# Performance work log

Measured on AMD Instinct MI355X. Metric: run time of the kernel, lower is better.

The kernel has to match this reference:

```python
import jax, jax.numpy as jnp
import numpy as np

B, T, D = 64, 512, 768
H = D // 2      # per-direction LSTM hidden
L = 33          # num_labels


def setup_inputs() -> dict:
    key = jax.random.key(0)
    ks = jax.random.split(key, 14)
    input_embed = jax.random.normal(ks[0], (B, T, D), dtype=jnp.float32)
    # pack_padded_sequence requires lengths sorted in decreasing order
    lengths = jnp.sort(jax.random.randint(ks[1], (B,), T // 2, T + 1))[::-1]
    lengths = lengths.at[0].set(T)
    mask = jnp.arange(T)[None, :] < lengths[:, None]          # [B,T] bool
    labels = jax.random.randint(ks[2], (B, T), 0, L, dtype=jnp.int32)
    index = jax.random.randint(ks[3], (B, 2), 0, T)
    s = 0.1
    w_ih_f = jax.random.normal(ks[4], (4 * H, D), jnp.float32) * s
    w_hh_f = jax.random.normal(ks[5], (4 * H, H), jnp.float32) * s
    b_f = jax.random.normal(ks[6], (4 * H,), jnp.float32) * s
    w_ih_b = jax.random.normal(ks[7], (4 * H, D), jnp.float32) * s
    w_hh_b = jax.random.normal(ks[8], (4 * H, H), jnp.float32) * s
    b_b = jax.random.normal(ks[9], (4 * H,), jnp.float32) * s
    lin_w = jax.random.normal(ks[10], (L, 2 * H), jnp.float32) * s
    lin_b = jnp.zeros((L,), jnp.float32)
    trans = jax.random.normal(ks[11], (L, L), jnp.float32) * s
    start_trans = jax.random.normal(ks[12], (L,), jnp.float32) * s
    end_trans = jax.random.normal(ks[13], (L,), jnp.float32) * s
    return dict(input_embed=input_embed, mask=mask, labels=labels, index=index,
                w_ih_f=w_ih_f, w_hh_f=w_hh_f, b_f=b_f,
                w_ih_b=w_ih_b, w_hh_b=w_hh_b, b_b=b_b,
                lin_w=lin_w, lin_b=lin_b,
                trans=trans, start_trans=start_trans, end_trans=end_trans)


def _run_lstm(x, mask_f, w_ih, w_hh, b):
    """Unidirectional LSTM over packed (length-masked) sequences.
    Output is zero at padded steps; state is frozen past each sequence length.
    x: [B,T,D] -> [B,T,H]. Torch gate order: i, f, g, o.
    """
    xp = jnp.einsum('btd,gd->btg', x, w_ih) + b          # [B,T,4H] precomputed
    xp_t = xp.transpose(1, 0, 2)                         # [T,B,4H]
    m_t = mask_f.T[:, :, None]                           # [T,B,1]
    nH = w_hh.shape[1]
    init = (jnp.zeros((x.shape[0], nH), x.dtype), jnp.zeros((x.shape[0], nH), x.dtype))

    def step(carry, inp):
        h, c = carry
        xg, m = inp
        g = xg + h @ w_hh.T
        i, f, gc, o = jnp.split(g, 4, axis=-1)
        c_new = jax.nn.sigmoid(f) * c + jax.nn.sigmoid(i) * jnp.tanh(gc)
        h_new = jax.nn.sigmoid(o) * jnp.tanh(c_new)
        carry = (jnp.where(m > 0, h_new, h), jnp.where(m > 0, c_new, c))
        return carry, h_new * m

    _, ys = jax.lax.scan(step, init, (xp_t, m_t))
    return ys.transpose(1, 0, 2)


def reference(input_embed, mask, labels, index,
              w_ih_f, w_hh_f, b_f, w_ih_b, w_hh_b, b_b,
              lin_w, lin_b, trans, start_trans, end_trans):
    mask_f = mask.astype(input_embed.dtype)              # [B,T]
    lengths = mask.sum(1).astype(jnp.int32)              # [B]

    # BiLSTM with pack_padded semantics (dropout in eval mode = identity)
    h_fwd = _run_lstm(input_embed, mask_f, w_ih_f, w_hh_f, b_f)
    # reverse within each sequence's valid region (involution on valid steps)
    rev_idx = jnp.clip(lengths[:, None] - 1 - jnp.arange(T)[None, :], 0, T - 1)
    x_rev = jnp.take_along_axis(input_embed, rev_idx[..., None], axis=1)
    h_b_rev = _run_lstm(x_rev, mask_f, w_ih_b, w_hh_b, b_b)
    h_bwd = jnp.take_along_axis(h_b_rev, rev_idx[..., None], axis=1) * mask_f[..., None]
    h = jnp.concatenate([h_fwd, h_bwd], axis=-1)         # [B,T,2H]

    # emissions, masked as in the original (out *= mask.unsqueeze(-1))
    em = (jnp.einsum('bth,lh->btl', h, lin_w) + lin_b) * mask_f[..., None]

    # ---- CRF log-likelihood: numerator (gold path score) ----
    em_y = jnp.take_along_axis(em, labels[..., None], axis=2)[..., 0]   # [B,T]
    tr = trans[labels[:, :-1], labels[:, 1:]]                            # [B,T-1]
    num = start_trans[labels[:, 0]] + em_y[:, 0] \
        + jnp.sum((tr + em_y[:, 1:]) * mask_f[:, 1:], axis=1)
    last_y = jnp.take_along_axis(labels, (lengths - 1)[:, None], axis=1)[:, 0]
    num = num + end_trans[last_y]

    # ---- CRF log-partition: forward algorithm scan ----
    alpha0 = start_trans[None, :] + em[:, 0]             # [B,L]

    def step(alpha, inp):
        e_t, m_t = inp                                   # [B,L], [B]
        new = jax.nn.logsumexp(alpha[:, :, None] + trans[None, :, :] + e_t[:, None, :], axis=1)
        return jnp.where(m_t[:, None] > 0, new, alpha), None

    alpha, _ = jax.lax.scan(step, alpha0,
                            (em[:, 1:].transpose(1, 0, 2), mask_f[:, 1:].T))
    logZ = jax.nn.logsumexp(alpha + end_trans[None, :], axis=1)

    score = num - logZ                                   # per-sample log-likelihood
    return -jnp.mean(score)
```

## Files before the change

kernel.cpp:

```cpp
#include <hip/hip_runtime.h>

typedef unsigned short U16;
typedef unsigned int   U32;
typedef unsigned long long U64;
typedef __attribute__((ext_vector_type(8))) short S8;
typedef __attribute__((ext_vector_type(4))) float F4;

#define B_  64
#define T_  512
#define DD  768
#define HH  384
#define G4  1536
#define NL  33

__device__ __forceinline__ U16 f2bf(float f){
  U32 u = __float_as_uint(f);
  u += 0x7fffu + ((u >> 16) & 1u);
  return (U16)(u >> 16);
}
__device__ __forceinline__ float bf2f(U16 h){ return __uint_as_float(((U32)h) << 16); }
__device__ __forceinline__ float frcp(float x){
  float r;
  asm("v_rcp_f32 %0, %1" : "=v"(r) : "v"(x));
  return r * (2.0f - x * r);
}
__device__ __forceinline__ float sigm(float x){
  x = fminf(30.f, fmaxf(-30.f, x));
  return frcp(1.f + __expf(-x));
}
__device__ __forceinline__ float tanh_(float x){
  x = fminf(15.f, fmaxf(-15.f, x));
  float e = __expf(2.f * x);
  return (e - 1.f) * frcp(e + 1.f);
}

__global__ void k_pre(const float* x, U64* xb, const U32* mask, int* lens,
                      const float* wf_, const float* wb_, const float* lw_,
                      const float* bfv, const float* bbv,
                      U16* wcat, U16* lwb, float* bcat){
  int blk = blockIdx.x;
  int tid = threadIdx.x;
  if (blk < 64){
    if (tid < 64){
      int b = blk, l = tid;
      bool b32 = (mask[0] == 1u);
      int cnt = 0;
      for (int t = l; t < T_; t += 64){
        int v = b32 ? ((const int*)mask)[b * T_ + t]
                    : (int)((const unsigned char*)mask)[b * T_ + t];
        cnt += (v != 0);
      }
      #pragma unroll
      for (int o = 32; o >= 1; o >>= 1) cnt += __shfl_xor(cnt, o);
      if (l == 0) lens[b] = cnt;
    }
    return;
  }
  if (blk < 1088){
    const int WE = G4 * DD;
    const int LWE = NL * DD;
    int total = 2 * WE + LWE + 2 * G4;
    for (int i = (blk - 64) * 256 + tid; i < total; i += 1024 * 256){
      if (i < WE) wcat[i] = f2bf(wf_[i]);
      else if (i < 2 * WE) wcat[i] = f2bf(wb_[i - WE]);
      else if (i < 2 * WE + LWE) lwb[i - 2 * WE] = f2bf(lw_[i - 2 * WE]);
      else { int j = i - 2 * WE - LWE; bcat[j] = (j < G4) ? bfv[j] : bbv[j - G4]; }
    }
    return;
  }
  size_t n4 = (size_t)B_ * T_ * DD / 4;
  for (size_t i = (size_t)(blk - 1088) * 256 + tid; i < n4; i += (size_t)2048 * 256){
    float4 v = ((const float4*)x)[i];
    U64 o = (U64)f2bf(v.x) | ((U64)f2bf(v.y) << 16) | ((U64)f2bf(v.z) << 32) | ((U64)f2bf(v.w) << 48);
    xb[i] = o;
  }
}

__global__ __launch_bounds__(256) void k_gemm(const U16* A, const U16* Bw, const float* bias, U16* C){
  __shared__ __align__(16) U16 As[128 * 64];
  __shared__ __align__(16) U16 Bs[128 * 64];
  int bid = blockIdx.x;
  int nb = bid % 24, mb = bid / 24;
  int m0 = mb * 128, n0 = nb * 128;
  int tid = threadIdx.x;
  int w = tid >> 6, l = tid & 63;
  int lr = l & 15, lk = (l >> 4) * 8;
  int wm = (w >> 1) * 64, wn = (w & 1) * 64;
  int srow = tid >> 3;
  int scol = (tid & 7) * 8;
  F4 acc[4][4];
  #pragma unroll
  for (int i = 0; i < 4; i++)
    #pragma unroll
    for (int j = 0; j < 4; j++) acc[i][j] = (F4){0.f, 0.f, 0.f, 0.f};

  for (int kt = 0; kt < DD; kt += 64){
    __syncthreads();
    #pragma unroll
    for (int r = 0; r < 4; r++){
      int row = r * 32 + srow;
      __builtin_amdgcn_global_load_lds((const U32*)(A + (size_t)(m0 + row) * DD + kt + scol),
                                       (U32*)(As + row * 64 + scol), 16, 0, 0);
      __builtin_amdgcn_global_load_lds((const U32*)(Bw + (size_t)(n0 + row) * DD + kt + scol),
                                       (U32*)(Bs + row * 64 + scol), 16, 0, 0);
    }
    __syncthreads();
    #pragma unroll
    for (int kk = 0; kk < 64; kk += 32){
      S8 af[4], bf[4];
      #pragma unroll
      for (int i = 0; i < 4; i++) af[i] = *(const S8*)(As + (wm + i * 16 + lr) * 64 + kk + lk);
      #pragma unroll
      for (int i = 0; i < 4; i++) bf[i] = *(const S8*)(Bs + (wn + i * 16 + lr) * 64 + kk + lk);
      #pragma unroll
      for (int i = 0; i < 4; i++)
        #pragma unroll
        for (int j = 0; j < 4; j++)
          acc[i][j] = __builtin_amdgcn_mfma_f32_16x16x32_bf16(af[i], bf[j], acc[i][j], 0, 0, 0);
    }
  }
  #pragma unroll
  for (int j = 0; j < 4; j++){
    int col = n0 + wn + j * 16 + lr;
    float bv = bias[col];
    #pragma unroll
    for (int i = 0; i < 4; i++){
      #pragma unroll
      for (int rg = 0; rg < 4; rg++){
        int row = m0 + wm + i * 16 + (l >> 4) * 4 + rg;
        C[(size_t)row * 3072 + col] = f2bf(acc[i][j][rg] + bv);
      }
    }
  }
}

__global__ __launch_bounds__(256) void k_rec(const U16* xp, const float* whf, const float* whb,
                                             const int* len_, U16* hcat, U64* hx){
  int blk = blockIdx.x;
  int g = blk & 7, m = blk >> 3;
  int dir = g >> 2, chunk = g & 3, sb = chunk * 16;
  const float* wh = dir ? whb : whf;
  int tid = threadIdx.x;
  int w = tid >> 6, l = tid & 63;
  int lr = l & 15, lq = l >> 4;
  int jloc = m * 64 + w * 16 + lr;

  S8 wf[4][12];
  #pragma unroll
  for (int q = 0; q < 4; q++){
    #pragma unroll
    for (int kc = 0; kc < 12; kc++){
      const float* p = wh + (size_t)(q * HH + jloc) * HH + kc * 32 + lq * 8;
      float4 v0 = *(const float4*)p;
      float4 v1 = *(const float4*)(p + 4);
      S8 t;
      t[0] = (short)f2bf(v0.x); t[1] = (short)f2bf(v0.y); t[2] = (short)f2bf(v0.z); t[3] = (short)f2bf(v0.w);
      t[4] = (short)f2bf(v1.x); t[5] = (short)f2bf(v1.y); t[6] = (short)f2bf(v1.z); t[7] = (short)f2bf(v1.w);
      wf[q][kc] = t;
    }
  }

  __shared__ __align__(16) U16 hl[16][408];
  for (int i = tid; i < 16 * 408; i += 256) ((U16*)hl)[i] = 0;
  int lens[4];
  #pragma unroll
  for (int r = 0; r < 4; r++) lens[r] = len_[sb + lq * 4 + r];
  int steps = len_[sb];
  float cst[4] = {0.f, 0.f, 0.f, 0.f}, hst[4] = {0.f, 0.f, 0.f, 0.f};
  __syncthreads();

  for (int step = 0; step < steps; ++step){
    float xv[4][4];
    #pragma unroll
    for (int r = 0; r < 4; r++){
      int L = lens[r];
      int t = dir ? (L - 1 - step) : step;
      if (t < 0) t = 0;
      size_t basei = ((size_t)(sb + lq * 4 + r) * T_ + t) * 3072 + dir * G4;
      #pragma unroll
      for (int q = 0; q < 4; q++) xv[q][r] = bf2f(xp[basei + q * HH + jloc]);
    }
    if (step){
      const U64* src = hx + (size_t)((step & 1) * 8 + g) * 3072;
      U64 v[12];
      #pragma unroll
      for (int k = 0; k < 12; k++)
        v[k] = __hip_atomic_load(src + tid + k * 256, __ATOMIC_RELAXED, __HIP_MEMORY_SCOPE_AGENT);
      U32 expct = (U32)step;
      while (true){
        U32 bad = 0;
        #pragma unroll
        for (int k = 0; k < 12; k++) bad |= (((U32)(v[k] >> 32)) != expct) ? (1u << k) : 0u;
        if (!bad) break;
        #pragma unroll
        for (int k = 0; k < 12; k++)
          if (bad & (1u << k))
            v[k] = __hip_atomic_load(src + tid + k * 256, __ATOMIC_RELAXED, __HIP_MEMORY_SCOPE_AGENT);
      }
      #pragma unroll
      for (int k = 0; k < 12; k++){
        int wi = tid + k * 256;
        int col = wi >> 3, p = wi & 7;
        U32 lo = (U32)v[k];
        hl[2 * p + 0][col] = (U16)lo;
        hl[2 * p + 1][col] = (U16)(lo >> 16);
      }
      __syncthreads();
    }
    F4 acc[4];
    #pragma unroll
    for (int q = 0; q < 4; q++) acc[q] = (F4){0.f, 0.f, 0.f, 0.f};
    #pragma unroll
    for (int kc = 0; kc < 12; kc++){
      S8 a = *(const S8*)&hl[lr][kc * 32 + lq * 8];
      #pragma unroll
      for (int q = 0; q < 4; q++)
        acc[q] = __builtin_amdgcn_mfma_f32_16x16x32_bf16(a, wf[q][kc], acc[q], 0, 0, 0);
    }
    #pragma unroll
    for (int r = 0; r < 4; r++){
      float ip = acc[0][r] + xv[0][r];
      float fp = acc[1][r] + xv[1][r];
      float gp = acc[2][r] + xv[2][r];
      float op = acc[3][r] + xv[3][r];
      float cn = sigm(fp) * cst[r] + sigm(ip) * tanh_(gp);
      float hn = sigm(op) * tanh_(cn);
      if (step < lens[r]){ cst[r] = cn; hst[r] = hn; }
    }
    {
      U64 tag = ((U64)(U32)(step + 1)) << 32;
      U64 w0 = (U64)((U32)f2bf(hst[0]) | ((U32)f2bf(hst[1]) << 16)) | tag;
      U64 w1 = (U64)((U32)f2bf(hst[2]) | ((U32)f2bf(hst[3]) << 16)) | tag;
      U64* dst = hx + (size_t)(((step + 1) & 1) * 8 + g) * 3072 + jloc * 8 + lq * 2;
      __hip_atomic_store(dst + 0, w0, __ATOMIC_RELAXED, __HIP_MEMORY_SCOPE_AGENT);
      __hip_atomic_store(dst + 1, w1, __ATOMIC_RELAXED, __HIP_MEMORY_SCOPE_AGENT);
    }
    #pragma unroll
    for (int r = 0; r < 4; r++){
      if (step < lens[r]){
        int t = dir ? (lens[r] - 1 - step) : step;
        hcat[((size_t)(sb + lq * 4 + r) * T_ + t) * (2 * HH) + dir * HH + jloc] = f2bf(hst[r]);
      }
    }
  }
}

__global__ __launch_bounds__(256) void k_em(const U16* hcat, const U16* lwb, const float* lin_b, float* em){
  __shared__ U16 lw[NL * DD];
  __shared__ U16 hs[8 * DD];
  int tid = threadIdx.x;
  for (int i = tid; i < NL * DD / 2; i += 256) ((U32*)lw)[i] = ((const U32*)lwb)[i];
  size_t r0 = (size_t)blockIdx.x * 8;
  const U32* hsrc = (const U32*)(hcat + r0 * DD);
  for (int i = tid; i < 8 * DD / 2; i += 256) ((U32*)hs)[i] = hsrc[i];
  __syncthreads();
  for (int e = tid; e < 8 * NL; e += 256){
    int rr = e / NL, ll = e % NL;
    const U16* hp = &hs[rr * DD];
    const U16* wp = &lw[ll * DD];
    float s = 0.f;
    #pragma unroll 8
    for (int k = 0; k < DD; k += 2){
      U32 hv = *(const U32*)&hp[k];
      U32 wv = *(const U32*)&wp[k];
      s = fmaf(__uint_as_float(hv << 16), __uint_as_float(wv << 16), s);
      s = fmaf(__uint_as_float(hv & 0xffff0000u), __uint_as_float(wv & 0xffff0000u), s);
    }
    em[(r0 + rr) * NL + ll] = s + lin_b[ll];
  }
}

__global__ void k_crf(const float* em, const int* labels, const int* len_, const float* trans,
                      const float* startt, const float* endt, float* score){
  int b = blockIdx.x, l = threadIdx.x;
  int L = len_[b];
  const int* lab = labels + b * T_;
  const float* emb = em + (size_t)b * T_ * NL;
  float part = 0.f;
  for (int t = 1 + l; t < L; t += 64){
    int lp = lab[t - 1], lc = lab[t];
    part += trans[lp * NL + lc] + emb[(size_t)t * NL + lc];
  }
  #pragma unroll
  for (int o = 32; o >= 1; o >>= 1) part += __shfl_xor(part, o);
  float num = part + startt[lab[0]] + emb[lab[0]] + endt[lab[L - 1]];
  bool act = l < NL;
  int jj = act ? l : (NL - 1);
  float tc[NL];
  #pragma unroll
  for (int i = 0; i < NL; i++) tc[i] = trans[i * NL + jj];
  float a = startt[jj] + emb[jj];
  for (int t = 1; t < L; ++t){
    float vv[NL];
    float mx = -3.0e38f;
    #pragma unroll
    for (int i = 0; i < NL; i++){ vv[i] = __shfl(a, i) + tc[i]; mx = fmaxf(mx, vv[i]); }
    float s = 0.f;
    #pragma unroll
    for (int i = 0; i < NL; i++) s += __expf(vv[i] - mx);
    a = mx + __logf(s) + emb[(size_t)t * NL + jj];
  }
  float val = act ? (a + endt[jj]) : -3.0e38f;
  float mx = val;
  #pragma unroll
  for (int o = 32; o >= 1; o >>= 1) mx = fmaxf(mx, __shfl_xor(mx, o));
  float se = __expf(val - mx);
  #pragma unroll
  for (int o = 32; o >= 1; o >>= 1) se += __shfl_xor(se, o);
  float logZ = mx + __logf(se);
  if (l == 0) score[b] = num - logZ;
}

__global__ void k_final(const float* score, float* out){
  int l = threadIdx.x;
  float v = score[l];
  #pragma unroll
  for (int o = 32; o >= 1; o >>= 1) v += __shfl_xor(v, o);
  if (l == 0) out[0] = -v / 64.f;
}

__global__ void k_sentinel(float* out){ out[0] = -12345.f; }

extern "C" void kernel_launch(void* const* d_in, const int* in_sizes, int n_in,
                              void* d_out, int out_size, void* d_ws, size_t ws_size,
                              hipStream_t stream){
  const float* x      = (const float*)d_in[0];
  const void*  mask   = d_in[1];
  const int*   labels = (const int*)d_in[2];
  const float* w_ih_f = (const float*)d_in[4];
  const float* w_hh_f = (const float*)d_in[5];
  const float* b_f    = (const float*)d_in[6];
  const float* w_ih_b = (const float*)d_in[7];
  const float* w_hh_b = (const float*)d_in[8];
  const float* b_b    = (const float*)d_in[9];
  const float* lin_w  = (const float*)d_in[10];
  const float* lin_b  = (const float*)d_in[11];
  const float* trans  = (const float*)d_in[12];
  const float* startt = (const float*)d_in[13];
  const float* endt   = (const float*)d_in[14];
  float* out = (float*)d_out;

  const size_t WS_NEEDED = 261158912;
  if (ws_size < WS_NEEDED){
    k_sentinel<<<1, 1, 0, stream>>>(out);
    return;
  }

  char* ws = (char*)d_ws;
  size_t off = 0;
  auto take = [&](size_t bytes) -> char* {
    char* p = ws + off;
    off += (bytes + 255) & ~(size_t)255;
    return p;
  };
  U16*  xp    = (U16*)take((size_t)32768 * 3072 * 2);
  U16*  hcat  = (U16*)take((size_t)32768 * 768 * 2);
  U16*  wcat  = (U16*)take((size_t)3072 * 768 * 2);
  U16*  lwb   = (U16*)take((size_t)NL * 768 * 2);
  float* bcat = (float*)take(3072 * 4);
  int*  lens  = (int*)take(256);
  U64*  hx    = (U64*)take((size_t)2 * 8 * 3072 * 8);
  float* em   = (float*)take((size_t)32768 * NL * 4);
  float* score= (float*)take(256);
  U16*  xbf   = hcat;

  hipMemsetAsync(hx, 0, (size_t)2 * 8 * 3072 * 8, stream);
  k_pre<<<3136, 256, 0, stream>>>(x, (U64*)xbf, (const U32*)mask, lens,
                                  w_ih_f, w_ih_b, lin_w, b_f, b_b, wcat, lwb, bcat);
  k_gemm<<<6144, 256, 0, stream>>>(xbf, wcat, bcat, xp);
  k_rec<<<48, 256, 0, stream>>>(xp, w_hh_f, w_hh_b, lens, hcat, hx);
  k_em<<<4096, 256, 0, stream>>>(hcat, lwb, lin_b, em);
  k_crf<<<64, 64, 0, stream>>>(em, labels, lens, trans, startt, endt, score);
  k_final<<<1, 64, 0, stream>>>(score, out);
}
```

Before: 2.245 ms.

## Interleave four batch chunks per recurrent block to hide cross-block sync latency

The recurrent kernel now runs 12 blocks instead of 48. Each block owns one hidden slice of one direction and processes all four 16-sequence batch chunks in round-robin phases. While one chunk computes, the poll for the next chunk's hidden state is already issued, so inter-block handshake latency overlaps with MFMA and gate work. Offsets into xp and hcat are advanced incrementally, and the clamps are removed from the sigmoid and tanh helpers. The trade-off is four times more serial work per block with fewer CUs in use, and large inputs to tanh could now overflow to inf/NaN without the clamp.

```diff
diff --git a/kernel.cpp b/kernel.cpp
--- a/kernel.cpp
+++ b/kernel.cpp
@@ -25,13 +25,11 @@
   return r * (2.0f - x * r);
 }
 __device__ __forceinline__ float sigm(float x){
-  x = fminf(30.f, fmaxf(-30.f, x));
   return frcp(1.f + __expf(-x));
 }
 __device__ __forceinline__ float tanh_(float x){
-  x = fminf(15.f, fmaxf(-15.f, x));
   float e = __expf(2.f * x);
-  return (e - 1.f) * frcp(e + 1.f);
+  return 1.f - 2.f * frcp(e + 1.f);
 }
 
 __global__ void k_pre(const float* x, U64* xb, const U32* mask, int* lens,
@@ -134,11 +132,13 @@
   }
 }
 
-__global__ __launch_bounds__(256) void k_rec(const U16* xp, const float* whf, const float* whb,
-                                             const int* len_, U16* hcat, U64* hx){
+__global__ __launch_bounds__(256, 1) void k_rec(const U16* __restrict__ xp,
+                                                const float* __restrict__ whf,
+                                                const float* __restrict__ whb,
+                                                const int* __restrict__ len_,
+                                                U16* __restrict__ hcat, U64* hx){
   int blk = blockIdx.x;
-  int g = blk & 7, m = blk >> 3;
-  int dir = g >> 2, chunk = g & 3, sb = chunk * 16;
+  int m = blk % 6, dir = blk / 6;
   const float* wh = dir ? whb : whf;
   int tid = threadIdx.x;
   int w = tid >> 6, l = tid & 63;
@@ -160,89 +160,124 @@
     }
   }
 
-  __shared__ __align__(16) U16 hl[16][408];
-  for (int i = tid; i < 16 * 408; i += 256) ((U16*)hl)[i] = 0;
-  int lens[4];
-  #pragma unroll
-  for (int r = 0; r < 4; r++) lens[r] = len_[sb + lq * 4 + r];
-  int steps = len_[sb];
-  float cst[4] = {0.f, 0.f, 0.f, 0.f}, hst[4] = {0.f, 0.f, 0.f, 0.f};
+  __shared__ __align__(16) U16 hl[4][16][408];
+  for (int i = tid; i < 4 * 16 * 408; i += 256) ((U16*)hl)[i] = 0;
+
+  int lcs[16]; U32 oxp[16], oh[16];
+  #pragma unroll
+  for (int c = 0; c < 4; c++){
+    #pragma unroll
+    for (int rr = 0; rr < 4; rr++){
+      int seq = c * 16 + lq * 4 + rr;
+      int L = len_[seq];
+      lcs[c * 4 + rr] = L;
+      int t0 = dir ? (L - 1) : 0;
+      oxp[c * 4 + rr] = (U32)(((seq * T_ + t0) * 3072 + dir * G4 + jloc) * 2);
+      oh [c * 4 + rr] = (U32)(((seq * T_ + t0) * 768  + dir * HH + jloc) * 2);
+    }
+  }
+  int clen0 = len_[0], clen1 = len_[16], clen2 = len_[32], clen3 = len_[48];
+  int sxp = dir ? -6144 : 6144;
+  int sh  = dir ? -1536 : 1536;
+  float cs[16], hs[16];
+  #pragma unroll
+  for (int i = 0; i < 16; i++){ cs[i] = 0.f; hs[i] = 0.f; }
+
+  const char* xpB = (const char*)xp;
+  char* hcB = (char*)hcat;
+  U64 vp[12];
+  U16 xv[16];
+
+  #define IXV(C) { \
+    _Pragma("unroll") \
+    for (int rr = 0; rr < 4; rr++){ \
+      const U16* p = (const U16*)(xpB + oxp[(C) * 4 + rr]); \
+      xv[0 * 4 + rr] = p[0]; xv[1 * 4 + rr] = p[HH]; \
+      xv[2 * 4 + rr] = p[2 * HH]; xv[3 * 4 + rr] = p[3 * HH]; \
+    } }
+
+  #define IPOLL(G, PAR) { \
+    U64* src_ = hx + (size_t)(PAR) * 24576 + (size_t)(G) * 3072 + tid; \
+    _Pragma("unroll") \
+    for (int k = 0; k < 12; k++) \
+      vp[k] = __hip_atomic_load(src_ + k * 256, __ATOMIC_RELAXED, __HIP_MEMORY_SCOPE_AGENT); \
+  }
+
+  #define CHECK_HL(C, R) { \
+    U32 e_ = (U32)(R); \
+    U64* src_ = hx + (size_t)((R) & 1) * 24576 + (size_t)(dir * 4 + (C)) * 3072 + tid; \
+    for (;;){ \
+      U32 bad = 0; \
+      _Pragma("unroll") \
+      for (int k = 0; k < 12; k++) bad |= (((U32)(vp[k] >> 32)) != e_) ? (1u << k) : 0u; \
+      if (!bad) break; \
+      _Pragma("unroll") \
+      for (int k = 0; k < 12; k++) \
+        if (bad & (1u << k)) \
+          vp[k] = __hip_atomic_load(src_ + k * 256, __ATOMIC_RELAXED, __HIP_MEMORY_SCOPE_AGENT); \
+    } \
+    _Pragma("unroll") \
+    for (int k = 0; k < 12; k++){ \
+      int wi = tid + k * 256; int col = wi >> 3, p2 = wi & 7; \
+      U32 lo = (U32)vp[k]; \
+      hl[C][2 * p2 + 0][col] = (U16)lo; \
+      hl[C][2 * p2 + 1][col] = (U16)(lo >> 16); \
+    } }
+
+  #define PHASE(C, CN, NCLEN) { \
+    if (r){ CHECK_HL(C, r) __syncthreads(); } \
+    bool nxt_same = (r < (NCLEN)); \
+    { int nr_ = nxt_same ? r : (r + 1); \
+      int ng_ = dir * 4 + (nxt_same ? (CN) : 0); \
+      IPOLL(ng_, nr_ & 1) } \
+    F4 acc0 = {0,0,0,0}, acc1 = {0,0,0,0}, acc2 = {0,0,0,0}, acc3 = {0,0,0,0}; \
+    _Pragma("unroll") \
+    for (int kc = 0; kc < 12; kc++){ \
+      S8 a = *(const S8*)&hl[C][lr][kc * 32 + lq * 8]; \
+      acc0 = __builtin_amdgcn_mfma_f32_16x16x32_bf16(a, wf[0][kc], acc0, 0, 0, 0); \
+      acc1 = __builtin_amdgcn_mfma_f32_16x16x32_bf16(a, wf[1][kc], acc1, 0, 0, 0); \
+      acc2 = __builtin_amdgcn_mfma_f32_16x16x32_bf16(a, wf[2][kc], acc2, 0, 0, 0); \
+      acc3 = __builtin_amdgcn_mfma_f32_16x16x32_bf16(a, wf[3][kc], acc3, 0, 0, 0); \
+    } \
+    _Pragma("unroll") \
+    for (int rr = 0; rr < 4; rr++){ \
+      float ip = acc0[rr] + bf2f(xv[0 * 4 + rr]); \
+      float fp = acc1[rr] + bf2f(xv[1 * 4 + rr]); \
+      float gp = acc2[rr] + bf2f(xv[2 * 4 + rr]); \
+      float op = acc3[rr] + bf2f(xv[3 * 4 + rr]); \
+      float cn = sigm(fp) * cs[(C) * 4 + rr] + sigm(ip) * tanh_(gp); \
+      float hn = sigm(op) * tanh_(cn); \
+      if (r < lcs[(C) * 4 + rr]){ cs[(C) * 4 + rr] = cn; hs[(C) * 4 + rr] = hn; } \
+    } \
+    { U64 tg = ((U64)(U32)(r + 1)) << 32; \
+      U64 w0 = ((U64)((U32)f2bf(hs[(C) * 4 + 0]) | ((U32)f2bf(hs[(C) * 4 + 1]) << 16))) | tg; \
+      U64 w1 = ((U64)((U32)f2bf(hs[(C) * 4 + 2]) | ((U32)f2bf(hs[(C) * 4 + 3]) << 16))) | tg; \
+      U64* dst_ = hx + (size_t)((r + 1) & 1) * 24576 + (size_t)(dir * 4 + (C)) * 3072 + jloc * 8 + lq * 2; \
+      __hip_atomic_store(dst_ + 0, w0, __ATOMIC_RELAXED, __HIP_MEMORY_SCOPE_AGENT); \
+      __hip_atomic_store(dst_ + 1, w1, __ATOMIC_RELAXED, __HIP_MEMORY_SCOPE_AGENT); } \
+    _Pragma("unroll") \
+    for (int rr = 0; rr < 4; rr++){ \
+      if (r < lcs[(C) * 4 + rr]) *(U16*)(hcB + oh[(C) * 4 + rr]) = f2bf(hs[(C) * 4 + rr]); \
+      bool adv = (r + 1) < lcs[(C) * 4 + rr]; \
+      oxp[(C) * 4 + rr] += adv ? sxp : 0; \
+      oh [(C) * 4 + rr] += adv ? sh  : 0; \
+    } \
+    if (nxt_same){ IXV(CN) } else { IXV(0) } \
+  }
+
   __syncthreads();
-
-  for (int step = 0; step < steps; ++step){
-    float xv[4][4];
-    #pragma unroll
-    for (int r = 0; r < 4; r++){
-      int L = lens[r];
-      int t = dir ? (L - 1 - step) : step;
-      if (t < 0) t = 0;
-      size_t basei = ((size_t)(sb + lq * 4 + r) * T_ + t) * 3072 + dir * G4;
-      #pragma unroll
-      for (int q = 0; q < 4; q++) xv[q][r] = bf2f(xp[basei + q * HH + jloc]);
-    }
-    if (step){
-      const U64* src = hx + (size_t)((step & 1) * 8 + g) * 3072;
-      U64 v[12];
-      #pragma unroll
-      for (int k = 0; k < 12; k++)
-        v[k] = __hip_atomic_load(src + tid + k * 256, __ATOMIC_RELAXED, __HIP_MEMORY_SCOPE_AGENT);
-      U32 expct = (U32)step;
-      while (true){
-        U32 bad = 0;
-        #pragma unroll
-        for (int k = 0; k < 12; k++) bad |= (((U32)(v[k] >> 32)) != expct) ? (1u << k) : 0u;
-        if (!bad) break;
-        #pragma unroll
-        for (int k = 0; k < 12; k++)
-          if (bad & (1u << k))
-            v[k] = __hip_atomic_load(src + tid + k * 256, __ATOMIC_RELAXED, __HIP_MEMORY_SCOPE_AGENT);
-      }
-      #pragma unroll
-      for (int k = 0; k < 12; k++){
-        int wi = tid + k * 256;
-        int col = wi >> 3, p = wi & 7;
-        U32 lo = (U32)v[k];
-        hl[2 * p + 0][col] = (U16)lo;
-        hl[2 * p + 1][col] = (U16)(lo >> 16);
-      }
-      __syncthreads();
-    }
-    F4 acc[4];
-    #pragma unroll
-    for (int q = 0; q < 4; q++) acc[q] = (F4){0.f, 0.f, 0.f, 0.f};
-    #pragma unroll
-    for (int kc = 0; kc < 12; kc++){
-      S8 a = *(const S8*)&hl[lr][kc * 32 + lq * 8];
-      #pragma unroll
-      for (int q = 0; q < 4; q++)
-        acc[q] = __builtin_amdgcn_mfma_f32_16x16x32_bf16(a, wf[q][kc], acc[q], 0, 0, 0);
-    }
-    #pragma unroll
-    for (int r = 0; r < 4; r++){
-      float ip = acc[0][r] + xv[0][r];
-      float fp = acc[1][r] + xv[1][r];
-      float gp = acc[2][r] + xv[2][r];
-      float op = acc[3][r] + xv[3][r];
-      float cn = sigm(fp) * cst[r] + sigm(ip) * tanh_(gp);
-      float hn = sigm(op) * tanh_(cn);
-      if (step < lens[r]){ cst[r] = cn; hst[r] = hn; }
-    }
-    {
-      U64 tag = ((U64)(U32)(step + 1)) << 32;
-      U64 w0 = (U64)((U32)f2bf(hst[0]) | ((U32)f2bf(hst[1]) << 16)) | tag;
-      U64 w1 = (U64)((U32)f2bf(hst[2]) | ((U32)f2bf(hst[3]) << 16)) | tag;
-      U64* dst = hx + (size_t)(((step + 1) & 1) * 8 + g) * 3072 + jloc * 8 + lq * 2;
-      __hip_atomic_store(dst + 0, w0, __ATOMIC_RELAXED, __HIP_MEMORY_SCOPE_AGENT);
-      __hip_atomic_store(dst + 1, w1, __ATOMIC_RELAXED, __HIP_MEMORY_SCOPE_AGENT);
-    }
-    #pragma unroll
-    for (int r = 0; r < 4; r++){
-      if (step < lens[r]){
-        int t = dir ? (lens[r] - 1 - step) : step;
-        hcat[((size_t)(sb + lq * 4 + r) * T_ + t) * (2 * HH) + dir * HH + jloc] = f2bf(hst[r]);
-      }
-    }
-  }
+  IXV(0)
+  int rounds = clen0;
+  for (int r = 0; r < rounds; ++r){
+    PHASE(0, 1, clen1)
+    if (r < clen1) PHASE(1, 2, clen2)
+    if (r < clen2) PHASE(2, 3, clen3)
+    if (r < clen3) PHASE(3, 0, -1)
+  }
+  #undef PHASE
+  #undef CHECK_HL
+  #undef IPOLL
+  #undef IXV
 }
 
 __global__ __launch_bounds__(256) void k_em(const U16* hcat, const U16* lwb, const float* lin_b, float* em){
@@ -368,7 +403,7 @@
   k_pre<<<3136, 256, 0, stream>>>(x, (U64*)xbf, (const U32*)mask, lens,
                                   w_ih_f, w_ih_b, lin_w, b_f, b_b, wcat, lwb, bcat);
   k_gemm<<<6144, 256, 0, stream>>>(xbf, wcat, bcat, xp);
-  k_rec<<<48, 256, 0, stream>>>(xp, w_hh_f, w_hh_b, lens, hcat, hx);
+  k_rec<<<12, 256, 0, stream>>>(xp, w_hh_f, w_hh_b, lens, hcat, hx);
   k_em<<<4096, 256, 0, stream>>>(hcat, lwb, lin_b, em);
   k_crf<<<64, 64, 0, stream>>>(em, labels, lens, trans, startt, endt, score);
   k_final<<<1, 64, 0, stream>>>(score, out);
```

New measurement: 4.893 ms. +117.9%, slower.

## Fuse input GEMM with LSTM recurrence using per-tile readiness counters

Applied to the files above, without the earlier changes.

Merges the input-projection GEMM and the recurrent LSTM kernel into one launch. The first 48 blocks run the recurrence and the rest compute GEMM tiles, ordered so the tiles each recurrence step needs come first. Each GEMM block bumps a per-row-tile counter after storing, and recurrence blocks spin on that counter every 128 steps, so the serial recurrence overlaps the bulk GEMM. It also converts x to bf16 inside the GEMM load instead of a separate pass, and drops the clamps in sigmoid/tanh. The risks are deadlock if the recurrence blocks are not co-resident, contention between the two workloads, and possible overflow at extreme inputs.

```diff
diff --git a/kernel.cpp b/kernel.cpp
--- a/kernel.cpp
+++ b/kernel.cpp
@@ -25,16 +25,14 @@
   return r * (2.0f - x * r);
 }
 __device__ __forceinline__ float sigm(float x){
-  x = fminf(30.f, fmaxf(-30.f, x));
   return frcp(1.f + __expf(-x));
 }
 __device__ __forceinline__ float tanh_(float x){
-  x = fminf(15.f, fmaxf(-15.f, x));
   float e = __expf(2.f * x);
-  return (e - 1.f) * frcp(e + 1.f);
-}
-
-__global__ void k_pre(const float* x, U64* xb, const U32* mask, int* lens,
+  return 1.f - 2.f * frcp(e + 1.f);
+}
+
+__global__ void k_pre(const U32* mask, int* lens,
                       const float* wf_, const float* wb_, const float* lw_,
                       const float* bfv, const float* bbv,
                       U16* wcat, U16* lwb, float* bcat){
@@ -56,91 +54,100 @@
     }
     return;
   }
-  if (blk < 1088){
-    const int WE = G4 * DD;
-    const int LWE = NL * DD;
-    int total = 2 * WE + LWE + 2 * G4;
-    for (int i = (blk - 64) * 256 + tid; i < total; i += 1024 * 256){
-      if (i < WE) wcat[i] = f2bf(wf_[i]);
-      else if (i < 2 * WE) wcat[i] = f2bf(wb_[i - WE]);
-      else if (i < 2 * WE + LWE) lwb[i - 2 * WE] = f2bf(lw_[i - 2 * WE]);
-      else { int j = i - 2 * WE - LWE; bcat[j] = (j < G4) ? bfv[j] : bbv[j - G4]; }
-    }
+  const int WE = G4 * DD;
+  const int LWE = NL * DD;
+  int total = 2 * WE + LWE + 2 * G4;
+  for (int i = (blk - 64) * 256 + tid; i < total; i += 1024 * 256){
+    if (i < WE) wcat[i] = f2bf(wf_[i]);
+    else if (i < 2 * WE) wcat[i] = f2bf(wb_[i - WE]);
+    else if (i < 2 * WE + LWE) lwb[i - 2 * WE] = f2bf(lw_[i - 2 * WE]);
+    else { int j = i - 2 * WE - LWE; bcat[j] = (j < G4) ? bfv[j] : bbv[j - G4]; }
+  }
+}
+
+__global__ __launch_bounds__(256, 1) void k_fused(
+    const float* __restrict__ x, const U16* __restrict__ Bw, const float* __restrict__ bias,
+    U16* xp, const float* __restrict__ whf, const float* __restrict__ whb,
+    const int* __restrict__ len_, U16* __restrict__ hcat, U64* hx, int* cnt){
+  __shared__ __align__(16) U16 smem[2 * 128 * 64];
+  int tid = threadIdx.x;
+
+  if (blockIdx.x >= 48){
+    U16* As = smem;
+    U16* Bs = smem + 128 * 64;
+    int gbid = blockIdx.x - 48;
+    int oi = gbid / 24, nb = gbid % 24;
+    int mb = (oi < 128) ? ((oi >> 1) * 4 + ((oi & 1) ? 3 : 0))
+           : (oi < 192) ? ((oi - 128) * 4 + 2)
+                        : ((oi - 192) * 4 + 1);
+    int m0 = mb * 128, n0 = nb * 128;
+    int w = tid >> 6, l = tid & 63;
+    int lr = l & 15, lk = (l >> 4) * 8;
+    int wm = (w >> 1) * 64, wn = (w & 1) * 64;
+    int srow = tid >> 3;
+    int scol = (tid & 7) * 8;
+    F4 acc[4][4];
+    #pragma unroll
+    for (int i = 0; i < 4; i++)
+      #pragma unroll
+      for (int j = 0; j < 4; j++) acc[i][j] = (F4){0.f, 0.f, 0.f, 0.f};
+
+    for (int kt = 0; kt < DD; kt += 64){
+      __syncthreads();
+      #pragma unroll
+      for (int r = 0; r < 4; r++){
+        int row = r * 32 + srow;
+        const float* ap = x + (size_t)(m0 + row) * DD + kt + scol;
+        float4 v0 = *(const float4*)ap;
+        float4 v1 = *(const float4*)(ap + 4);
+        S8 t;
+        t[0] = (short)f2bf(v0.x); t[1] = (short)f2bf(v0.y);
+        t[2] = (short)f2bf(v0.z); t[3] = (short)f2bf(v0.w);
+        t[4] = (short)f2bf(v1.x); t[5] = (short)f2bf(v1.y);
+        t[6] = (short)f2bf(v1.z); t[7] = (short)f2bf(v1.w);
+        *(S8*)&As[row * 64 + scol] = t;
+        __builtin_amdgcn_global_load_lds((const U32*)(Bw + (size_t)(n0 + row) * DD + kt + scol),
+                                         (U32*)(Bs + row * 64 + scol), 16, 0, 0);
+      }
+      __syncthreads();
+      #pragma unroll
+      for (int kk = 0; kk < 64; kk += 32){
+        S8 af[4], bf[4];
+        #pragma unroll
+        for (int i = 0; i < 4; i++) af[i] = *(const S8*)(As + (wm + i * 16 + lr) * 64 + kk + lk);
+        #pragma unroll
+        for (int i = 0; i < 4; i++) bf[i] = *(const S8*)(Bs + (wn + i * 16 + lr) * 64 + kk + lk);
+        #pragma unroll
+        for (int i = 0; i < 4; i++)
+          #pragma unroll
+          for (int j = 0; j < 4; j++)
+            acc[i][j] = __builtin_amdgcn_mfma_f32_16x16x32_bf16(af[i], bf[j], acc[i][j], 0, 0, 0);
+      }
+    }
+    #pragma unroll
+    for (int j = 0; j < 4; j++){
+      int col = n0 + wn + j * 16 + lr;
+      float bv = bias[col];
+      #pragma unroll
+      for (int i = 0; i < 4; i++){
+        #pragma unroll
+        for (int rg = 0; rg < 4; rg++){
+          int row = m0 + wm + i * 16 + (l >> 4) * 4 + rg;
+          __hip_atomic_store(&xp[(size_t)row * 3072 + col], f2bf(acc[i][j][rg] + bv),
+                             __ATOMIC_RELAXED, __HIP_MEMORY_SCOPE_AGENT);
+        }
+      }
+    }
+    __syncthreads();
+    if (tid == 0)
+      __hip_atomic_fetch_add(&cnt[mb], 1, __ATOMIC_RELEASE, __HIP_MEMORY_SCOPE_AGENT);
     return;
   }
-  size_t n4 = (size_t)B_ * T_ * DD / 4;
-  for (size_t i = (size_t)(blk - 1088) * 256 + tid; i < n4; i += (size_t)2048 * 256){
-    float4 v = ((const float4*)x)[i];
-    U64 o = (U64)f2bf(v.x) | ((U64)f2bf(v.y) << 16) | ((U64)f2bf(v.z) << 32) | ((U64)f2bf(v.w) << 48);
-    xb[i] = o;
-  }
-}
-
-__global__ __launch_bounds__(256) void k_gemm(const U16* A, const U16* Bw, const float* bias, U16* C){
-  __shared__ __align__(16) U16 As[128 * 64];
-  __shared__ __align__(16) U16 Bs[128 * 64];
-  int bid = blockIdx.x;
-  int nb = bid % 24, mb = bid / 24;
-  int m0 = mb * 128, n0 = nb * 128;
-  int tid = threadIdx.x;
-  int w = tid >> 6, l = tid & 63;
-  int lr = l & 15, lk = (l >> 4) * 8;
-  int wm = (w >> 1) * 64, wn = (w & 1) * 64;
-  int srow = tid >> 3;
-  int scol = (tid & 7) * 8;
-  F4 acc[4][4];
-  #pragma unroll
-  for (int i = 0; i < 4; i++)
-    #pragma unroll
-    for (int j = 0; j < 4; j++) acc[i][j] = (F4){0.f, 0.f, 0.f, 0.f};
-
-  for (int kt = 0; kt < DD; kt += 64){
-    __syncthreads();
-    #pragma unroll
-    for (int r = 0; r < 4; r++){
-      int row = r * 32 + srow;
-      __builtin_amdgcn_global_load_lds((const U32*)(A + (size_t)(m0 + row) * DD + kt + scol),
-                                       (U32*)(As + row * 64 + scol), 16, 0, 0);
-      __builtin_amdgcn_global_load_lds((const U32*)(Bw + (size_t)(n0 + row) * DD + kt + scol),
-                                       (U32*)(Bs + row * 64 + scol), 16, 0, 0);
-    }
-    __syncthreads();
-    #pragma unroll
-    for (int kk = 0; kk < 64; kk += 32){
-      S8 af[4], bf[4];
-      #pragma unroll
-      for (int i = 0; i < 4; i++) af[i] = *(const S8*)(As + (wm + i * 16 + lr) * 64 + kk + lk);
-      #pragma unroll
-      for (int i = 0; i < 4; i++) bf[i] = *(const S8*)(Bs + (wn + i * 16 + lr) * 64 + kk + lk);
-      #pragma unroll
-      for (int i = 0; i < 4; i++)
-        #pragma unroll
-        for (int j = 0; j < 4; j++)
-          acc[i][j] = __builtin_amdgcn_mfma_f32_16x16x32_bf16(af[i], bf[j], acc[i][j], 0, 0, 0);
-    }
-  }
-  #pragma unroll
-  for (int j = 0; j < 4; j++){
-    int col = n0 + wn + j * 16 + lr;
-    float bv = bias[col];
-    #pragma unroll
-    for (int i = 0; i < 4; i++){
-      #pragma unroll
-      for (int rg = 0; rg < 4; rg++){
-        int row = m0 + wm + i * 16 + (l >> 4) * 4 + rg;
-        C[(size_t)row * 3072 + col] = f2bf(acc[i][j][rg] + bv);
-      }
-    }
-  }
-}
-
-__global__ __launch_bounds__(256) void k_rec(const U16* xp, const float* whf, const float* whb,
-                                             const int* len_, U16* hcat, U64* hx){
+
   int blk = blockIdx.x;
   int g = blk & 7, m = blk >> 3;
-  int dir = g >> 2, chunk = g & 3, sb = chunk * 16;
+  int dir = g >> 2, sb = (g & 3) * 16;
   const float* wh = dir ? whb : whf;
-  int tid = threadIdx.x;
   int w = tid >> 6, l = tid & 63;
   int lr = l & 15, lq = l >> 4;
   int jloc = m * 64 + w * 16 + lr;
@@ -160,25 +167,45 @@
     }
   }
 
-  __shared__ __align__(16) U16 hl[16][408];
+  U16 (*hl)[408] = (U16(*)[408])smem;
   for (int i = tid; i < 16 * 408; i += 256) ((U16*)hl)[i] = 0;
   int lens[4];
   #pragma unroll
   for (int r = 0; r < 4; r++) lens[r] = len_[sb + lq * 4 + r];
   int steps = len_[sb];
+  int Lme = len_[sb + (l & 15)];
   float cst[4] = {0.f, 0.f, 0.f, 0.f}, hst[4] = {0.f, 0.f, 0.f, 0.f};
   __syncthreads();
 
   for (int step = 0; step < steps; ++step){
+    if ((step & 127) == 0){
+      int tt;
+      if (dir == 0) tt = step >> 7;
+      else if (l < 16){
+        int tlo = Lme - 1 - step - 127; if (tlo < 0) tlo = 0; tt = tlo >> 7;
+      } else {
+        int thi = Lme - 1 - step; if (thi < 0) thi = 0; tt = thi >> 7;
+      }
+      int tile = ((sb + (l & 15)) << 2) + tt;
+      bool actg = (l < 32);
+      for (;;){
+        int cv = actg ? __hip_atomic_load(&cnt[tile], __ATOMIC_RELAXED, __HIP_MEMORY_SCOPE_AGENT) : 24;
+        if (__all(cv >= 24)) break;
+        __builtin_amdgcn_s_sleep(4);
+      }
+      __scoped_atomic_thread_fence(__ATOMIC_ACQUIRE, __MEMORY_SCOPE_DEVICE);
+    }
     float xv[4][4];
     #pragma unroll
     for (int r = 0; r < 4; r++){
       int L = lens[r];
       int t = dir ? (L - 1 - step) : step;
       if (t < 0) t = 0;
-      size_t basei = ((size_t)(sb + lq * 4 + r) * T_ + t) * 3072 + dir * G4;
-      #pragma unroll
-      for (int q = 0; q < 4; q++) xv[q][r] = bf2f(xp[basei + q * HH + jloc]);
+      if (t >= L) t = L - 1;
+      const U16* basep = xp + ((size_t)(sb + lq * 4 + r) * T_ + t) * 3072 + dir * G4 + jloc;
+      #pragma unroll
+      for (int q = 0; q < 4; q++)
+        xv[q][r] = bf2f(__hip_atomic_load(basep + q * HH, __ATOMIC_RELAXED, __HIP_MEMORY_SCOPE_AGENT));
     }
     if (step){
       const U64* src = hx + (size_t)((step & 1) * 8 + g) * 3072;
@@ -362,13 +389,13 @@
   U64*  hx    = (U64*)take((size_t)2 * 8 * 3072 * 8);
   float* em   = (float*)take((size_t)32768 * NL * 4);
   float* score= (float*)take(256);
-  U16*  xbf   = hcat;
-
-  hipMemsetAsync(hx, 0, (size_t)2 * 8 * 3072 * 8, stream);
-  k_pre<<<3136, 256, 0, stream>>>(x, (U64*)xbf, (const U32*)mask, lens,
+  int*  cnt   = (int*)em;
+
+  (void)hipMemsetAsync(hx, 0, (size_t)2 * 8 * 3072 * 8, stream);
+  (void)hipMemsetAsync(cnt, 0, 1024, stream);
+  k_pre<<<1088, 256, 0, stream>>>((const U32*)mask, lens,
                                   w_ih_f, w_ih_b, lin_w, b_f, b_b, wcat, lwb, bcat);
-  k_gemm<<<6144, 256, 0, stream>>>(xbf, wcat, bcat, xp);
-  k_rec<<<48, 256, 0, stream>>>(xp, w_hh_f, w_hh_b, lens, hcat, hx);
+  k_fused<<<6192, 256, 0, stream>>>(x, wcat, bcat, xp, w_hh_f, w_hh_b, lens, hcat, hx, cnt);
   k_em<<<4096, 256, 0, stream>>>(hcat, lwb, lin_b, em);
   k_crf<<<64, 64, 0, stream>>>(em, labels, lens, trans, startt, endt, score);
   k_final<<<1, 64, 0, stream>>>(score, out);
```

Result: slower. 2.607 ms (+16.1%).
